# Optimization experiments

Measured on AMD Instinct MI355X. Metric: run time of the kernel, lower is better.

Reference implementation:

```python
import jax, jax.numpy as jnp
import numpy as np

B, N, C, H = 16, 4096, 384, 8
D = C // H  # head_dim = 48
WSTD = 0.02


def setup_inputs() -> dict:
    key = jax.random.key(0)
    ks = jax.random.split(key, 9)
    return {
        "x": jax.random.normal(ks[0], (B, N, C), dtype=jnp.float32),
        "conv_w": jax.random.normal(ks[1], (C, C), dtype=jnp.float32) * WSTD,  # Conv1d k=1, squeezed
        "conv_b": jax.random.normal(ks[2], (C,), dtype=jnp.float32) * WSTD,
        "wq": jax.random.normal(ks[3], (C, C), dtype=jnp.float32) * WSTD,
        "bq": jax.random.normal(ks[4], (C,), dtype=jnp.float32) * WSTD,
        "wkv": jax.random.normal(ks[5], (2 * C, C), dtype=jnp.float32) * WSTD,
        "bkv": jax.random.normal(ks[6], (2 * C,), dtype=jnp.float32) * WSTD,
        "wp": jax.random.normal(ks[7], (C, C), dtype=jnp.float32) * WSTD,
        "bp": jax.random.normal(ks[8], (C,), dtype=jnp.float32) * WSTD,
    }


def reference(x, conv_w, conv_b, wq, bq, wkv, bkv, wp, bp):
    b, n, c = x.shape
    h, d = H, c // H
    # Conv1d kernel_size=1 over channels == per-token linear: y = x @ W^T + b
    x_in = jnp.einsum("bnc,oc->bno", x, conv_w) + conv_b  # [B,N,C]
    # q: reshape(B,N,1,H,d).permute(2,0,3,4,1)[0] -> [B,H,d,N]
    q = (x_in @ wq.T + bq).reshape(b, n, h, d).transpose(0, 2, 3, 1)  # [B,H,d,N]
    kv = (x_in @ wkv.T + bkv).reshape(b, n, 2, h, d).transpose(2, 0, 3, 4, 1)  # [2,B,H,d,N]
    k, v = kv[0], kv[1]
    scale = jnp.asarray(n, x.dtype) ** -0.5  # note: N^-0.5, not head_dim^-0.5
    attn = jax.nn.softmax((q * scale) @ jnp.swapaxes(k, -2, -1), axis=-1)  # [B,H,d,d]
    out = attn @ v  # [B,H,d,N]
    # transpose(1,2) -> [B,d,H,N], then raw reshape to [B,N,C] (verbatim torch layout)
    out = jnp.transpose(out, (0, 2, 1, 3)).reshape(b, n, c)
    return out @ wp.T + bp
```

## Files before the change

### kernel.cpp

```cpp
#include <hip/hip_runtime.h>
#include <hip/hip_bf16.h>
#include <stdint.h>

#define DEVI static __device__ __forceinline__

typedef __attribute__((ext_vector_type(4))) float f32x4;
typedef __attribute__((ext_vector_type(8))) short bf16x8;
typedef unsigned short u16;
typedef unsigned int u32;
typedef unsigned long long u64;

#define BB 16
#define NN 4096
#define CC 384
#define HH 8
#define DD 48

DEVI u16 f2bf(float f) {
  union { float f; u32 u; } c; c.f = f;
  u32 u = c.u;
  u32 r = (u + 0x7FFFu + ((u >> 16) & 1u)) >> 16;
  return (u16)r;
}
DEVI float bf2f(u16 h) {
  union { float f; u32 u; } c; c.u = ((u32)h) << 16;
  return c.f;
}
DEVI void stage8(u16* dst, const float* src) {
  const f32x4 a = *(const f32x4*)(src);
  const f32x4 b = *(const f32x4*)(src + 4);
  union { bf16x8 v; u16 u[8]; } o;
  o.u[0] = f2bf(a[0]); o.u[1] = f2bf(a[1]); o.u[2] = f2bf(a[2]); o.u[3] = f2bf(a[3]);
  o.u[4] = f2bf(b[0]); o.u[5] = f2bf(b[1]); o.u[6] = f2bf(b[2]); o.u[7] = f2bf(b[3]);
  *(bf16x8*)dst = o.v;
}

typedef const __attribute__((address_space(1))) void* gas_ptr;
typedef __attribute__((address_space(3))) void* las_ptr;
DEVI void gload16(const void* g, void* l) {
  __builtin_amdgcn_global_load_lds((gas_ptr)g, (las_ptr)l, 16, 0, 0);
}

__global__ __launch_bounds__(256)
void f32_to_bf16(const float* __restrict__ in, u16* __restrict__ out, int n8) {
  const int i = blockIdx.x * 256 + threadIdx.x;
  if (i >= n8) return;
  u16 tmp[8];
  stage8(tmp, in + (size_t)i * 8);
  *(bf16x8*)(out + (size_t)i * 8) = *(bf16x8*)tmp;
}

__global__ __launch_bounds__(256)
void convert_x(const float* __restrict__ x, u16* __restrict__ xb,
               u16* __restrict__ xbT) {
  __shared__ u32 LtT[64 * 33];
  const int ct = blockIdx.x, nt = blockIdx.y, b = blockIdx.z;
  const int t = threadIdx.x;
  const int n0 = nt * 64, c0 = ct * 64;
  const int cl = (t & 15) * 4;
  const int np = t >> 4;
#pragma unroll
  for (int pass = 0; pass < 2; ++pass) {
    const int w = np + pass * 16;
    const int n = w * 2;
    const float* s0 = &x[((size_t)(b * NN + n0 + n)) * CC + c0 + cl];
    const f32x4 a = *(const f32x4*)s0;
    const f32x4 bv = *(const f32x4*)(s0 + CC);
    const u16 a0 = f2bf(a[0]), a1 = f2bf(a[1]), a2 = f2bf(a[2]), a3 = f2bf(a[3]);
    const u16 b0 = f2bf(bv[0]), b1 = f2bf(bv[1]), b2 = f2bf(bv[2]), b3 = f2bf(bv[3]);
    *(u64*)&xb[((size_t)(b * NN + n0 + n)) * CC + c0 + cl] =
        (u64)a0 | ((u64)a1 << 16) | ((u64)a2 << 32) | ((u64)a3 << 48);
    *(u64*)&xb[((size_t)(b * NN + n0 + n + 1)) * CC + c0 + cl] =
        (u64)b0 | ((u64)b1 << 16) | ((u64)b2 << 32) | ((u64)b3 << 48);
    LtT[(cl + 0) * 33 + w] = (u32)a0 | ((u32)b0 << 16);
    LtT[(cl + 1) * 33 + w] = (u32)a1 | ((u32)b1 << 16);
    LtT[(cl + 2) * 33 + w] = (u32)a2 | ((u32)b2 << 16);
    LtT[(cl + 3) * 33 + w] = (u32)a3 | ((u32)b3 << 16);
  }
  __syncthreads();
#pragma unroll
  for (int pass = 0; pass < 2; ++pass) {
    const int v = pass * 256 + t;
    const int c = v >> 3, ng = v & 7;
    union { bf16x8 o; u32 q[4]; } u;
#pragma unroll
    for (int r = 0; r < 4; ++r) u.q[r] = LtT[c * 33 + ng * 4 + r];
    *(bf16x8*)&xbT[((size_t)(b * CC + c0 + c)) * NN + n0 + ng * 8] = u.o;
  }
}

__global__ __launch_bounds__(256)
void transpose_cw(const float* __restrict__ cw, u16* __restrict__ cwT) {
  __shared__ u32 LtT[64 * 33];
  const int mt = blockIdx.x, ct = blockIdx.y;
  const int t = threadIdx.x;
  const int m0 = mt * 64, c0 = ct * 64;
  const int cl = (t & 15) * 4;
  const int mp = t >> 4;
#pragma unroll
  for (int pass = 0; pass < 2; ++pass) {
    const int w = mp + pass * 16;
    const int m = w * 2;
    const float* s0 = &cw[(size_t)(m0 + m) * CC + c0 + cl];
    const f32x4 a = *(const f32x4*)s0;
    const f32x4 bv = *(const f32x4*)(s0 + CC);
#pragma unroll
    for (int i = 0; i < 4; ++i)
      LtT[(cl + i) * 33 + w] = (u32)f2bf(a[i]) | ((u32)f2bf(bv[i]) << 16);
  }
  __syncthreads();
#pragma unroll
  for (int pass = 0; pass < 2; ++pass) {
    const int v = pass * 256 + t;
    const int c = v >> 3, mg = v & 7;
    union { bf16x8 o; u32 q[4]; } u;
#pragma unroll
    for (int r = 0; r < 4; ++r) u.q[r] = LtT[c * 33 + mg * 4 + r];
    *(bf16x8*)&cwT[(size_t)(c0 + c) * CC + m0 + mg * 8] = u.o;
  }
}

__global__ __launch_bounds__(256)
void bias_fuse(const float* __restrict__ wq, const float* __restrict__ bq,
               const float* __restrict__ wkv, const float* __restrict__ bkv,
               const float* __restrict__ cb, float* __restrict__ bf_) {
  const int o = blockIdx.x * 4 + (threadIdx.x >> 6);
  const int lane = threadIdx.x & 63;
  const float* wrow;
  float b0;
  if (o < CC) { wrow = wq + (size_t)o * CC;        b0 = bq[o]; }
  else        { wrow = wkv + (size_t)(o - CC) * CC; b0 = bkv[o - CC]; }
  float s = 0.f;
  for (int m = lane; m < CC; m += 64) s += wrow[m] * cb[m];
#pragma unroll
  for (int off = 32; off; off >>= 1) s += __shfl_xor(s, off, 64);
  if (lane == 0) bf_[o] = b0 + s;
}

__global__ __launch_bounds__(256)
void colsum(const u16* __restrict__ xbT, float* __restrict__ sx) {
  const int b = blockIdx.y, c = blockIdx.x * 16 + (threadIdx.x >> 4);
  const int sl = threadIdx.x & 15;
  const u16* src = xbT + ((size_t)(b * CC + c)) * NN + sl * 256;
  float s = 0.f;
  for (int i = 0; i < 32; ++i) {
    const bf16x8 v = *(const bf16x8*)(src + i * 8);
#pragma unroll
    for (int r = 0; r < 8; ++r) s += bf2f((u16)v[r]);
  }
#pragma unroll
  for (int m = 1; m < 16; m <<= 1) s += __shfl_xor(s, m, 64);
  if (sl == 0) sx[b * CC + c] = s;
}

__global__ __launch_bounds__(128)
void proj_sx(const u16* __restrict__ Wf, const float* __restrict__ sx,
             float* __restrict__ P) {
  __shared__ float sl[CC];
  const int b = blockIdx.y, o = blockIdx.x * 128 + threadIdx.x;
  for (int i = threadIdx.x; i < CC; i += 128) sl[i] = sx[b * CC + i];
  __syncthreads();
  float acc = 0.f;
  const u16* wr = Wf + (size_t)o * CC;
  for (int c8 = 0; c8 < CC; c8 += 8) {
    const bf16x8 w = *(const bf16x8*)(wr + c8);
#pragma unroll
    for (int r = 0; r < 8; ++r) acc += bf2f((u16)w[r]) * sl[c8 + r];
  }
  P[b * 768 + o] = acc;
}

template<typename OT, int BIASMODE, int TRI = 0, int SWZ = 1>
__global__ __launch_bounds__(256)
void gemm_f(const u16* __restrict__ A, const u16* __restrict__ W,
            const float* __restrict__ bias, OT* __restrict__ C,
            int M, int N, int K, int klen, int nbn, int nbm, int tpb,
            long sA, long sW, long sC, long sCp, long sBias) {
  constexpr int BK = 64;
  __shared__ __align__(16) u16 smem[32768];

  const int nx = gridDim.x;
  const int lin = blockIdx.x;
  const int lin2 = SWZ ? (lin & 7) * (nx >> 3) + (lin >> 3) : lin;
  const int b = lin2 / tpb;
  int t2 = lin2 % tpb;
  int bn, bm, p;
  if constexpr (TRI) {
    const int tl = t2 % 6; p = t2 / 6;
    bm = tl < 3 ? 0 : (tl < 5 ? 1 : 2);
    bn = tl < 3 ? tl : (tl < 5 ? tl - 2 : 2);
  } else {
    bn = t2 % nbn; t2 /= nbn;
    bm = t2 % nbm;
    p = t2 / nbm;
  }
  A += (size_t)b * sA; W += (size_t)b * sW;
  C += (size_t)b * sC + (size_t)p * sCp;
  if (BIASMODE) bias += (size_t)b * sBias;

  const int t = threadIdx.x;
  const int wid = t >> 6, lane = t & 63;
  const int wr = wid >> 1, wc = wid & 1;
  const int row0 = bm * 128, col0 = bn * 128;
  const int lrow = lane & 15;
  const int lswz = (lane & 7) << 3;
  const int kstart = p * klen;

  const int arow = t >> 3;
  const int scol = ((t & 7) ^ ((t >> 3) & 7)) * 8;
  const u16* Ag = A + (size_t)(row0 + arow) * K + scol;
  const u16* Wg = W + (size_t)(col0 + arow) * K + scol;

  f32x4 acc[4][4] = {};
  const int NT = klen >> 6;

  auto stage = [&](int buf, int kt) {
    u16* Al = smem + buf * 16384 + t * 8;
    u16* Bl = smem + buf * 16384 + 8192 + t * 8;
    const int k0 = kstart + kt * BK;
#pragma unroll
    for (int it = 0; it < 4; ++it) {
      gload16(Ag + (size_t)(it * 32) * K + k0, Al + it * 2048);
      gload16(Wg + (size_t)(it * 32) * K + k0, Bl + it * 2048);
    }
  };

  stage(0, 0);
  __syncthreads();
  int cur = 0;
  for (int kt = 0; kt < NT; ++kt) {
    if (kt + 1 < NT) stage(cur ^ 1, kt + 1);
    const u16* As = smem + cur * 16384;
    const u16* Bs = smem + cur * 16384 + 8192;
#pragma unroll
    for (int kk = 0; kk < 2; ++kk) {
      const int lk = (kk * 32 + (lane >> 4) * 8) ^ lswz;
      bf16x8 af[4], bf[4];
#pragma unroll
      for (int i = 0; i < 4; ++i)
        af[i] = *(const bf16x8*)&As[(wr * 64 + i * 16 + lrow) * BK + lk];
#pragma unroll
      for (int j = 0; j < 4; ++j)
        bf[j] = *(const bf16x8*)&Bs[(wc * 64 + j * 16 + lrow) * BK + lk];
#pragma unroll
      for (int i = 0; i < 4; ++i)
#pragma unroll
        for (int j = 0; j < 4; ++j)
          acc[i][j] = __builtin_amdgcn_mfma_f32_16x16x32_bf16(af[i], bf[j], acc[i][j], 0, 0, 0);
    }
    __syncthreads();
    cur ^= 1;
  }

  const int lr = (lane >> 4) * 4;
  if constexpr (sizeof(OT) == 2) {
    u16* Ct = smem;
#pragma unroll
    for (int i = 0; i < 4; ++i)
#pragma unroll
      for (int j = 0; j < 4; ++j) {
        const int ccol = wc * 64 + j * 16 + lrow;
        float bv = 0.f;
        if constexpr (BIASMODE == 1) bv = bias[col0 + ccol];
#pragma unroll
        for (int r = 0; r < 4; ++r) {
          const int rrow = wr * 64 + i * 16 + lr + r;
          float b2 = bv;
          if constexpr (BIASMODE == 2) b2 = bias[row0 + rrow];
          Ct[rrow * 132 + ccol] = f2bf(acc[i][j][r] + b2);
        }
      }
    __syncthreads();
#pragma unroll
    for (int it = 0; it < 8; ++it) {
      const int id = it * 256 + t;
      const int row = id >> 4, c16 = (id & 15) * 8;
      *(bf16x8*)((u16*)C + (size_t)(row0 + row) * N + col0 + c16) =
          *(const bf16x8*)&Ct[row * 132 + c16];
    }
  } else {
    const int orow = row0 + wr * 64, ocol = col0 + wc * 64;
#pragma unroll
    for (int i = 0; i < 4; ++i)
#pragma unroll
      for (int j = 0; j < 4; ++j) {
        const int cc2 = ocol + j * 16 + lrow;
        float bv = 0.f;
        if constexpr (BIASMODE == 1) bv = bias[cc2];
#pragma unroll
        for (int r = 0; r < 4; ++r) {
          const int rr = orow + i * 16 + lr + r;
          float b2 = bv;
          if constexpr (BIASMODE == 2) b2 = bias[rr];
          C[(size_t)rr * N + cc2] = acc[i][j][r] + b2;
        }
      }
  }
}

__global__ __launch_bounds__(256)
void reduceG(const float* __restrict__ Gp, u16* __restrict__ Gbf) {
  const int b = blockIdx.y;
  const int e = blockIdx.x * 256 + threadIdx.x;
  const int i = e / CC, j = e % CC;
  const int ee = (i <= j) ? e : (j * CC + i);
  const float* s = Gp + (size_t)b * 4 * 147456 + ee;
  Gbf[(size_t)b * 147456 + e] =
      f2bf(s[0] + s[147456] + s[2 * 147456] + s[3 * 147456]);
}

__global__ __launch_bounds__(256)
void s_softmax(const u16* __restrict__ M1g, const u16* __restrict__ Wf,
               const float* __restrict__ bf_, const float* __restrict__ P,
               const u16* __restrict__ UvT, u16* __restrict__ AUb,
               float* __restrict__ rbias) {
  __shared__ float Sf[48 * 52];
  __shared__ __align__(16) u16 att[48 * 56];
  const int bh = blockIdx.x, b = bh >> 3, h = bh & 7;
  const int t = threadIdx.x, wid = t >> 6, lane = t & 63;
  const int lrow = lane & 15, lkq = lane >> 4;

  if (wid < 3) {
    f32x4 acc[3] = {};
    const u16* Arow = M1g + (size_t)b * 147456 + (size_t)(h * 48 + wid * 16 + lrow) * CC;
    const u16* Brow = Wf + (size_t)(CC + h * 48) * CC;
    for (int ks = 0; ks < 12; ++ks) {
      const int k = ks * 32 + lkq * 8;
      const bf16x8 af = *(const bf16x8*)(Arow + k);
#pragma unroll
      for (int j = 0; j < 3; ++j) {
        const bf16x8 bfr = *(const bf16x8*)(Brow + (size_t)(j * 16 + lrow) * CC + k);
        acc[j] = __builtin_amdgcn_mfma_f32_16x16x32_bf16(af, bfr, acc[j], 0, 0, 0);
      }
    }
    const int lr = lkq * 4;
#pragma unroll
    for (int j = 0; j < 3; ++j)
#pragma unroll
      for (int r = 0; r < 4; ++r)
        Sf[(wid * 16 + lr + r) * 52 + j * 16 + lrow] = acc[j][r];
  }
  __syncthreads();

  if (t < 48) {
    const float bi = bf_[h * 48 + t];
    const float pq = P[b * 768 + h * 48 + t];
    float row[48];
    float mx = -1e30f;
#pragma unroll
    for (int j = 0; j < 48; ++j) {
      const float g = bf_[CC + h * 48 + j];
      const float pk = P[b * 768 + CC + h * 48 + j];
      const float s = (Sf[t * 52 + j] + bi * pk + pq * g + 4096.f * bi * g) * 0.015625f;
      row[j] = s;
      mx = fmaxf(mx, s);
    }
    float sum = 0.f;
#pragma unroll
    for (int j = 0; j < 48; ++j) { row[j] = __expf(row[j] - mx); sum += row[j]; }
    const float inv = 1.f / sum;
    float rb = 0.f;
#pragma unroll
    for (int j = 0; j < 48; ++j) {
      const float a = row[j] * inv;
      att[t * 56 + j] = f2bf(a);
      rb += a * bf_[2 * CC + h * 48 + j];
    }
#pragma unroll
    for (int j = 48; j < 56; ++j) att[t * 56 + j] = 0;
    rbias[b * CC + t * 8 + h] = rb;
  }
  __syncthreads();

  f32x4 acc[3][6] = {};
  const u16* Vbase = UvT + h * 48;
  const bf16x8 z = {};
#pragma unroll
  for (int kk = 0; kk < 2; ++kk) {
    const int k = kk * 32 + lkq * 8;
    bf16x8 af[3];
#pragma unroll
    for (int i = 0; i < 3; ++i) {
      af[i] = *(const bf16x8*)&att[(i * 16 + lrow) * 56 + k];
      if (k >= 48) af[i] = z;
    }
#pragma unroll
    for (int ct = 0; ct < 6; ++ct) {
      const int c = wid * 96 + ct * 16 + lrow;
      bf16x8 bfr = *(const bf16x8*)(Vbase + (size_t)c * CC + k);
      if (k >= 48) bfr = z;
#pragma unroll
      for (int i = 0; i < 3; ++i)
        acc[i][ct] = __builtin_amdgcn_mfma_f32_16x16x32_bf16(af[i], bfr, acc[i][ct], 0, 0, 0);
    }
  }
  const int lr = lkq * 4;
#pragma unroll
  for (int i = 0; i < 3; ++i)
#pragma unroll
    for (int ct = 0; ct < 6; ++ct) {
      const int c = wid * 96 + ct * 16 + lrow;
#pragma unroll
      for (int r = 0; r < 4; ++r) {
        const int ii = i * 16 + lr + r;
        AUb[(size_t)b * 147456 + (size_t)(ii * 8 + h) * CC + c] = f2bf(acc[i][ct][r]);
      }
    }
}

extern "C" void kernel_launch(void* const* d_in, const int* in_sizes, int n_in,
                              void* d_out, int out_size, void* d_ws, size_t ws_size,
                              hipStream_t stream) {
  const float* x      = (const float*)d_in[0];
  const float* conv_w = (const float*)d_in[1];
  const float* conv_b = (const float*)d_in[2];
  const float* wq     = (const float*)d_in[3];
  const float* bq     = (const float*)d_in[4];
  const float* wkv    = (const float*)d_in[5];
  const float* bkv    = (const float*)d_in[6];
  const float* wp     = (const float*)d_in[7];
  const float* bp     = (const float*)d_in[8];
  float* y = (float*)d_out;

  char* ws = (char*)d_ws;
  u16*   Wf    = (u16*)(ws + 0);
  float* bf_   = (float*)(ws + 884736);
  u16*   wpb   = (u16*)(ws + 889344);
  u16*   UvT   = (u16*)(ws + 1184256);
  float* sx    = (float*)(ws + 1479168);
  float* P     = (float*)(ws + 1503744);
  float* rb    = (float*)(ws + 1552896);
  u16*   M1g   = (u16*)(ws + 1577472);
  u16*   Gbf   = (u16*)(ws + 6296064);
  u16*   AUb   = (u16*)(ws + 11014656);
  float* Gpart = (float*)(ws + 15733248);
  u16*   wtopb = (u16*)(ws + 53481984);
  u16*   cwTb  = (u16*)(ws + 54366720);
  u16*   xb    = (u16*)(ws + 54661632);
  u16*   xbT   = (u16*)(ws + 104993280);
  u16*   R     = xbT;

  convert_x<<<dim3(6, 64, 16), dim3(256), 0, stream>>>(x, xb, xbT);
  f32_to_bf16<<<dim3(72), dim3(256), 0, stream>>>(wp, wpb, (CC * CC) / 8);
  f32_to_bf16<<<dim3(72), dim3(256), 0, stream>>>(wq, wtopb, (CC * CC) / 8);
  f32_to_bf16<<<dim3(144), dim3(256), 0, stream>>>(wkv, wtopb + CC * CC,
                                                   (2 * CC * CC) / 8);
  transpose_cw<<<dim3(6, 6), dim3(256), 0, stream>>>(conv_w, cwTb);
  bias_fuse<<<dim3(288), dim3(256), 0, stream>>>(wq, bq, wkv, bkv, conv_b, bf_);
  gemm_f<u16, 0, 0, 0><<<dim3(18), dim3(256), 0, stream>>>(
      wtopb, cwTb, nullptr, Wf, 2 * CC, CC, CC, CC, 3, 6, 18,
      0, 0, 0, 0, 0);
  gemm_f<u16, 0, 0, 0><<<dim3(9), dim3(256), 0, stream>>>(
      cwTb, wtopb + 2 * CC * CC, nullptr, UvT, CC, CC, CC, CC, 3, 3, 9,
      0, 0, 0, 0, 0);
  colsum<<<dim3(24, 16), dim3(256), 0, stream>>>(xbT, sx);
  proj_sx<<<dim3(6, 16), dim3(128), 0, stream>>>(Wf, sx, P);
  gemm_f<float, 0, 1><<<dim3(384), dim3(256), 0, stream>>>(
      xbT, xbT, nullptr, Gpart, CC, CC, NN, 1024, 3, 3, 24,
      (long)CC * NN, (long)CC * NN, 4L * 147456, 147456, 0);
  reduceG<<<dim3(576, 16), dim3(256), 0, stream>>>(Gpart, Gbf);
  gemm_f<u16, 0><<<dim3(144), dim3(256), 0, stream>>>(
      Wf, Gbf, nullptr, M1g, CC, CC, CC, CC, 3, 3, 9,
      0, 147456, 147456, 0, 0);
  s_softmax<<<dim3(128), dim3(256), 0, stream>>>(M1g, Wf, bf_, P, UvT, AUb, rb);
  gemm_f<u16, 2><<<dim3(1536), dim3(256), 0, stream>>>(
      AUb, xb, rb, R, CC, NN, CC, CC, 32, 3, 96,
      147456, (long)NN * CC, (long)NN * CC, 0, CC);
  gemm_f<float, 1><<<dim3(1536), dim3(256), 0, stream>>>(
      R, wpb, bp, y, BB * NN, CC, CC, CC, 3, 512, 1536,
      0, 0, 0, 0, 0);
}
```

Baseline: 225.1 us.

## Use 512-thread GEMM blocks with 8 waves and widen convert_x tiles

The GEMM kernel moves from 4 waves (2x2, each 64x64) to 8 waves (2x4, each 64x32) per 128x128 tile. Each thread holds half the accumulators and issues half the staging loads, which should raise latency hiding and occupancy. Separately, convert_x now handles 128 tokens per block with 8-wide vector loads and stores and an XOR-swizzled LDS transpose that allows 16-byte reads. Risks: each wave reuses less of the B fragment per MFMA, and 512-thread blocks may reduce how many blocks fit per CU.

Result: no change. 223.2 us (-0.8%).

```diff
diff --git a/kernel.cpp b/kernel.cpp
--- a/kernel.cpp
+++ b/kernel.cpp
@@ -5,6 +5,7 @@
 #define DEVI static __device__ __forceinline__
 
 typedef __attribute__((ext_vector_type(4))) float f32x4;
+typedef __attribute__((ext_vector_type(4))) unsigned int u32x4;
 typedef __attribute__((ext_vector_type(8))) short bf16x8;
 typedef unsigned short u16;
 typedef unsigned int u32;
@@ -53,39 +54,49 @@
 __global__ __launch_bounds__(256)
 void convert_x(const float* __restrict__ x, u16* __restrict__ xb,
                u16* __restrict__ xbT) {
-  __shared__ u32 LtT[64 * 33];
+  __shared__ u32 LtT[64 * 68];
   const int ct = blockIdx.x, nt = blockIdx.y, b = blockIdx.z;
   const int t = threadIdx.x;
-  const int n0 = nt * 64, c0 = ct * 64;
-  const int cl = (t & 15) * 4;
-  const int np = t >> 4;
-#pragma unroll
-  for (int pass = 0; pass < 2; ++pass) {
-    const int w = np + pass * 16;
-    const int n = w * 2;
-    const float* s0 = &x[((size_t)(b * NN + n0 + n)) * CC + c0 + cl];
-    const f32x4 a = *(const f32x4*)s0;
-    const f32x4 bv = *(const f32x4*)(s0 + CC);
-    const u16 a0 = f2bf(a[0]), a1 = f2bf(a[1]), a2 = f2bf(a[2]), a3 = f2bf(a[3]);
-    const u16 b0 = f2bf(bv[0]), b1 = f2bf(bv[1]), b2 = f2bf(bv[2]), b3 = f2bf(bv[3]);
-    *(u64*)&xb[((size_t)(b * NN + n0 + n)) * CC + c0 + cl] =
-        (u64)a0 | ((u64)a1 << 16) | ((u64)a2 << 32) | ((u64)a3 << 48);
-    *(u64*)&xb[((size_t)(b * NN + n0 + n + 1)) * CC + c0 + cl] =
-        (u64)b0 | ((u64)b1 << 16) | ((u64)b2 << 32) | ((u64)b3 << 48);
-    LtT[(cl + 0) * 33 + w] = (u32)a0 | ((u32)b0 << 16);
-    LtT[(cl + 1) * 33 + w] = (u32)a1 | ((u32)b1 << 16);
-    LtT[(cl + 2) * 33 + w] = (u32)a2 | ((u32)b2 << 16);
-    LtT[(cl + 3) * 33 + w] = (u32)a3 | ((u32)b3 << 16);
-  }
-  __syncthreads();
-#pragma unroll
-  for (int pass = 0; pass < 2; ++pass) {
-    const int v = pass * 256 + t;
-    const int c = v >> 3, ng = v & 7;
-    union { bf16x8 o; u32 q[4]; } u;
-#pragma unroll
-    for (int r = 0; r < 4; ++r) u.q[r] = LtT[c * 33 + ng * 4 + r];
-    *(bf16x8*)&xbT[((size_t)(b * CC + c0 + c)) * NN + n0 + ng * 8] = u.o;
+  const int n0 = nt * 128, c0 = ct * 64;
+  const int coct = t & 7, c = coct * 8;
+  const int q = t >> 3;
+
+  f32x4 v[2][4];
+#pragma unroll
+  for (int p = 0; p < 2; ++p) {
+    const int n = 2 * (p * 32 + q);
+    const float* s0 = &x[((size_t)(b * NN + n0 + n)) * CC + c0 + c];
+    v[p][0] = *(const f32x4*)s0;
+    v[p][1] = *(const f32x4*)(s0 + 4);
+    v[p][2] = *(const f32x4*)(s0 + CC);
+    v[p][3] = *(const f32x4*)(s0 + CC + 4);
+  }
+#pragma unroll
+  for (int p = 0; p < 2; ++p) {
+    const int npair = p * 32 + q;
+    const int n = 2 * npair;
+    union { bf16x8 o; u16 e[8]; } ua, ub;
+#pragma unroll
+    for (int r = 0; r < 4; ++r) {
+      ua.e[r] = f2bf(v[p][0][r]); ua.e[r + 4] = f2bf(v[p][1][r]);
+      ub.e[r] = f2bf(v[p][2][r]); ub.e[r + 4] = f2bf(v[p][3][r]);
+    }
+    *(bf16x8*)&xb[((size_t)(b * NN + n0 + n)) * CC + c0 + c] = ua.o;
+    *(bf16x8*)&xb[((size_t)(b * NN + n0 + n + 1)) * CC + c0 + c] = ub.o;
+    const int npw = npair ^ (coct << 3);
+#pragma unroll
+    for (int i = 0; i < 8; ++i)
+      LtT[(c + i) * 68 + npw] = (u32)ua.e[i] | ((u32)ub.e[i] << 16);
+  }
+  __syncthreads();
+#pragma unroll
+  for (int p = 0; p < 4; ++p) {
+    const int id = p * 256 + t;
+    const int cc2 = id >> 4, ng = id & 15;
+    const int co2 = (cc2 >> 3) & 7;
+    union { u32x4 q4; bf16x8 o; } u;
+    u.q4 = *(const u32x4*)&LtT[cc2 * 68 + ((ng * 4) ^ (co2 << 3))];
+    *(bf16x8*)&xbT[((size_t)(b * CC + c0 + cc2)) * NN + n0 + ng * 8] = u.o;
   }
 }
 
@@ -171,7 +182,7 @@
 }
 
 template<typename OT, int BIASMODE, int TRI = 0, int SWZ = 1>
-__global__ __launch_bounds__(256)
+__global__ __launch_bounds__(512)
 void gemm_f(const u16* __restrict__ A, const u16* __restrict__ W,
             const float* __restrict__ bias, OT* __restrict__ C,
             int M, int N, int K, int klen, int nbn, int nbm, int tpb,
@@ -200,7 +211,7 @@
 
   const int t = threadIdx.x;
   const int wid = t >> 6, lane = t & 63;
-  const int wr = wid >> 1, wc = wid & 1;
+  const int wr = wid >> 2, wc = wid & 3;
   const int row0 = bm * 128, col0 = bn * 128;
   const int lrow = lane & 15;
   const int lswz = (lane & 7) << 3;
@@ -211,7 +222,7 @@
   const u16* Ag = A + (size_t)(row0 + arow) * K + scol;
   const u16* Wg = W + (size_t)(col0 + arow) * K + scol;
 
-  f32x4 acc[4][4] = {};
+  f32x4 acc[4][2] = {};
   const int NT = klen >> 6;
 
   auto stage = [&](int buf, int kt) {
@@ -219,9 +230,9 @@
     u16* Bl = smem + buf * 16384 + 8192 + t * 8;
     const int k0 = kstart + kt * BK;
 #pragma unroll
-    for (int it = 0; it < 4; ++it) {
-      gload16(Ag + (size_t)(it * 32) * K + k0, Al + it * 2048);
-      gload16(Wg + (size_t)(it * 32) * K + k0, Bl + it * 2048);
+    for (int it = 0; it < 2; ++it) {
+      gload16(Ag + (size_t)(it * 64) * K + k0, Al + it * 4096);
+      gload16(Wg + (size_t)(it * 64) * K + k0, Bl + it * 4096);
     }
   };
 
@@ -235,18 +246,18 @@
 #pragma unroll
     for (int kk = 0; kk < 2; ++kk) {
       const int lk = (kk * 32 + (lane >> 4) * 8) ^ lswz;
-      bf16x8 af[4], bf[4];
+      bf16x8 af[4], bfv[2];
 #pragma unroll
       for (int i = 0; i < 4; ++i)
         af[i] = *(const bf16x8*)&As[(wr * 64 + i * 16 + lrow) * BK + lk];
 #pragma unroll
-      for (int j = 0; j < 4; ++j)
-        bf[j] = *(const bf16x8*)&Bs[(wc * 64 + j * 16 + lrow) * BK + lk];
+      for (int j = 0; j < 2; ++j)
+        bfv[j] = *(const bf16x8*)&Bs[(wc * 32 + j * 16 + lrow) * BK + lk];
 #pragma unroll
       for (int i = 0; i < 4; ++i)
 #pragma unroll
-        for (int j = 0; j < 4; ++j)
-          acc[i][j] = __builtin_amdgcn_mfma_f32_16x16x32_bf16(af[i], bf[j], acc[i][j], 0, 0, 0);
+        for (int j = 0; j < 2; ++j)
+          acc[i][j] = __builtin_amdgcn_mfma_f32_16x16x32_bf16(af[i], bfv[j], acc[i][j], 0, 0, 0);
     }
     __syncthreads();
     cur ^= 1;
@@ -258,8 +269,8 @@
 #pragma unroll
     for (int i = 0; i < 4; ++i)
 #pragma unroll
-      for (int j = 0; j < 4; ++j) {
-        const int ccol = wc * 64 + j * 16 + lrow;
+      for (int j = 0; j < 2; ++j) {
+        const int ccol = wc * 32 + j * 16 + lrow;
         float bv = 0.f;
         if constexpr (BIASMODE == 1) bv = bias[col0 + ccol];
 #pragma unroll
@@ -272,18 +283,18 @@
       }
     __syncthreads();
 #pragma unroll
-    for (int it = 0; it < 8; ++it) {
-      const int id = it * 256 + t;
+    for (int it = 0; it < 4; ++it) {
+      const int id = it * 512 + t;
       const int row = id >> 4, c16 = (id & 15) * 8;
       *(bf16x8*)((u16*)C + (size_t)(row0 + row) * N + col0 + c16) =
           *(const bf16x8*)&Ct[row * 132 + c16];
     }
   } else {
-    const int orow = row0 + wr * 64, ocol = col0 + wc * 64;
+    const int orow = row0 + wr * 64, ocol = col0 + wc * 32;
 #pragma unroll
     for (int i = 0; i < 4; ++i)
 #pragma unroll
-      for (int j = 0; j < 4; ++j) {
+      for (int j = 0; j < 2; ++j) {
         const int cc2 = ocol + j * 16 + lrow;
         float bv = 0.f;
         if constexpr (BIASMODE == 1) bv = bias[cc2];
@@ -440,33 +451,33 @@
   u16*   xbT   = (u16*)(ws + 104993280);
   u16*   R     = xbT;
 
-  convert_x<<<dim3(6, 64, 16), dim3(256), 0, stream>>>(x, xb, xbT);
+  convert_x<<<dim3(6, 32, 16), dim3(256), 0, stream>>>(x, xb, xbT);
   f32_to_bf16<<<dim3(72), dim3(256), 0, stream>>>(wp, wpb, (CC * CC) / 8);
   f32_to_bf16<<<dim3(72), dim3(256), 0, stream>>>(wq, wtopb, (CC * CC) / 8);
   f32_to_bf16<<<dim3(144), dim3(256), 0, stream>>>(wkv, wtopb + CC * CC,
                                                    (2 * CC * CC) / 8);
   transpose_cw<<<dim3(6, 6), dim3(256), 0, stream>>>(conv_w, cwTb);
   bias_fuse<<<dim3(288), dim3(256), 0, stream>>>(wq, bq, wkv, bkv, conv_b, bf_);
-  gemm_f<u16, 0, 0, 0><<<dim3(18), dim3(256), 0, stream>>>(
+  gemm_f<u16, 0, 0, 0><<<dim3(18), dim3(512), 0, stream>>>(
       wtopb, cwTb, nullptr, Wf, 2 * CC, CC, CC, CC, 3, 6, 18,
       0, 0, 0, 0, 0);
-  gemm_f<u16, 0, 0, 0><<<dim3(9), dim3(256), 0, stream>>>(
+  gemm_f<u16, 0, 0, 0><<<dim3(9), dim3(512), 0, stream>>>(
       cwTb, wtopb + 2 * CC * CC, nullptr, UvT, CC, CC, CC, CC, 3, 3, 9,
       0, 0, 0, 0, 0);
   colsum<<<dim3(24, 16), dim3(256), 0, stream>>>(xbT, sx);
   proj_sx<<<dim3(6, 16), dim3(128), 0, stream>>>(Wf, sx, P);
-  gemm_f<float, 0, 1><<<dim3(384), dim3(256), 0, stream>>>(
+  gemm_f<float, 0, 1><<<dim3(384), dim3(512), 0, stream>>>(
       xbT, xbT, nullptr, Gpart, CC, CC, NN, 1024, 3, 3, 24,
       (long)CC * NN, (long)CC * NN, 4L * 147456, 147456, 0);
   reduceG<<<dim3(576, 16), dim3(256), 0, stream>>>(Gpart, Gbf);
-  gemm_f<u16, 0><<<dim3(144), dim3(256), 0, stream>>>(
+  gemm_f<u16, 0><<<dim3(144), dim3(512), 0, stream>>>(
       Wf, Gbf, nullptr, M1g, CC, CC, CC, CC, 3, 3, 9,
       0, 147456, 147456, 0, 0);
   s_softmax<<<dim3(128), dim3(256), 0, stream>>>(M1g, Wf, bf_, P, UvT, AUb, rb);
-  gemm_f<u16, 2><<<dim3(1536), dim3(256), 0, stream>>>(
+  gemm_f<u16, 2><<<dim3(1536), dim3(512), 0, stream>>>(
       AUb, xb, rb, R, CC, NN, CC, CC, 32, 3, 96,
       147456, (long)NN * CC, (long)NN * CC, 0, CC);
-  gemm_f<float, 1><<<dim3(1536), dim3(256), 0, stream>>>(
+  gemm_f<float, 1><<<dim3(1536), dim3(512), 0, stream>>>(
       R, wpb, bp, y, BB * NN, CC, CC, CC, 3, 512, 1536,
       0, 0, 0, 0, 0);
 }
```
